# Kernel tuning notes

Hardware: AMD Instinct MI355X
Metric: run time of the kernel (lower is better)

## Reference

```python
import jax, jax.numpy as jnp
import numpy as np
import math

D_MODEL = 1024
N_HEADS = 16
D_KV = 64
NUM_BUCKETS = 32
MAX_DISTANCE = 128
BATCH = 4
SEQ = 2048


def _relative_position_bucket(relative_position, num_buckets=NUM_BUCKETS, max_distance=MAX_DISTANCE):
    # bidirectional=True (encoder)
    num_buckets //= 2
    relative_buckets = (relative_position > 0).astype(jnp.int32) * num_buckets
    rp = jnp.abs(relative_position)
    max_exact = num_buckets // 2
    is_small = rp < max_exact
    rp_safe = jnp.maximum(rp, 1)  # avoid log(0); masked by is_small anyway
    rp_if_large = max_exact + (
        jnp.log(rp_safe.astype(jnp.float32) / max_exact)
        / math.log(max_distance / max_exact)
        * (num_buckets - max_exact)
    ).astype(jnp.int32)
    rp_if_large = jnp.minimum(rp_if_large, num_buckets - 1)
    relative_buckets += jnp.where(is_small, rp, rp_if_large)
    return relative_buckets


def compute_bias(rel_bias, q_len, k_len):
    context = jnp.arange(q_len)[:, None]
    memory = jnp.arange(k_len)[None, :]
    buckets = _relative_position_bucket(memory - context)  # [q, k]
    values = rel_bias[buckets]                              # [q, k, h]
    return jnp.transpose(values, (2, 0, 1))[None]           # [1, h, q, k]


def setup_inputs() -> dict:
    key = jax.random.key(0)
    ks = jax.random.split(key, 6)
    s = 1.0 / math.sqrt(D_MODEL)
    return {
        "hidden_states": jax.random.normal(ks[0], (BATCH, SEQ, D_MODEL), jnp.float32),
        "wq": jax.random.normal(ks[1], (D_MODEL, N_HEADS * D_KV), jnp.float32) * s,
        "wk": jax.random.normal(ks[2], (D_MODEL, N_HEADS * D_KV), jnp.float32) * s,
        "wv": jax.random.normal(ks[3], (D_MODEL, N_HEADS * D_KV), jnp.float32) * s,
        "wo": jax.random.normal(ks[4], (N_HEADS * D_KV, D_MODEL), jnp.float32) * s,
        "rel_bias": jax.random.normal(ks[5], (NUM_BUCKETS, N_HEADS), jnp.float32) * 0.5,
    }


def reference(hidden_states, wq, wk, wv, wo, rel_bias):
    B, S, _ = hidden_states.shape

    def shape(x):  # [B,S,H*Dk] -> [B,H,S,Dk]
        return x.reshape(B, S, N_HEADS, D_KV).transpose(0, 2, 1, 3)

    q = shape(hidden_states @ wq)
    k = shape(hidden_states @ wk)
    v = shape(hidden_states @ wv)

    # NOTE: T5 does NOT scale by 1/sqrt(d_kv)
    scores = jnp.einsum("bhqd,bhkd->bhqk", q, k)
    position_bias = compute_bias(rel_bias, S, S)  # [1,H,S,S]
    scores = scores + position_bias
    attn = jax.nn.softmax(scores.astype(jnp.float32), axis=-1).astype(scores.dtype)
    ctx = jnp.einsum("bhqk,bhkd->bhqd", attn, v)
    ctx = ctx.transpose(0, 2, 1, 3).reshape(B, S, N_HEADS * D_KV)
    return ctx @ wo
```

## Files before the change

kernel.cpp:

```cpp
#include <hip/hip_runtime.h>
#include <hip/hip_bf16.h>

typedef unsigned short u16;
typedef unsigned int   u32;
typedef __bf16 bf16x8 __attribute__((ext_vector_type(8)));
typedef float  f32x4  __attribute__((ext_vector_type(4)));
typedef u16    u16x8  __attribute__((ext_vector_type(8)));
typedef u16    u16x4  __attribute__((ext_vector_type(4)));

#define MFMA16(a,b,c) __builtin_amdgcn_mfma_f32_16x16x32_bf16(a,b,c,0,0,0)
#define LOG2E 1.4426950408889634f

__device__ __forceinline__ u16 f2b(float f) {
    u32 u = __builtin_bit_cast(u32, f);
    u32 r = (u + 0x7FFFu + ((u >> 16) & 1u)) >> 16;
    return (u16)r;
}

typedef const __attribute__((address_space(1))) u32* gaddr_t;
typedef __attribute__((address_space(3))) u32*       laddr_t;
__device__ __forceinline__ void gl_lds16(const void* g, void* l) {
    __builtin_amdgcn_global_load_lds((gaddr_t)g, (laddr_t)l, 16, 0, 0);
}

__global__ __launch_bounds__(256) void prep_kernel(
        const float* __restrict__ H, const float* __restrict__ wq,
        const float* __restrict__ wk, const float* __restrict__ wv,
        const float* __restrict__ wo, const float* __restrict__ rel_bias,
        u16* __restrict__ Hb, u16* __restrict__ Wt, u16* __restrict__ Wot,
        float* __restrict__ tab) {
    __shared__ u16 tile[64 * 72];
    int bi = blockIdx.x;
    int t = threadIdx.x;
    if (bi < 4096) {
        int i = (bi * 256 + t) * 8;
        float4 a = *(const float4*)(H + i);
        float4 b = *(const float4*)(H + i + 4);
        u16x8 o = { f2b(a.x), f2b(a.y), f2b(a.z), f2b(a.w),
                    f2b(b.x), f2b(b.y), f2b(b.z), f2b(b.w) };
        *(u16x8*)(Hb + i) = o;
    } else if (bi < 5120) {
        int g2 = bi - 4096;
        int g = g2 >> 8, rem = g2 & 255;
        int n0 = (rem >> 4) * 64, k0 = (rem & 15) * 64;
        const float* src = (g == 0) ? wq : (g == 1) ? wk : (g == 2) ? wv : wo;
        u16* dst = (g < 3) ? (Wt + g * 1048576) : Wot;
#pragma unroll
        for (int rr = 0; rr < 4; ++rr) {
            int idx = rr * 256 + t;
            int kr = idx >> 4, c = idx & 15;
            float4 v = *(const float4*)(src + (k0 + kr) * 1024 + n0 + c * 4);
            u16x4 o = { f2b(v.x), f2b(v.y), f2b(v.z), f2b(v.w) };
            *(u16x4*)&tile[kr * 72 + c * 4] = o;
        }
        __syncthreads();
#pragma unroll
        for (int rr = 0; rr < 2; ++rr) {
            int idx = rr * 256 + t;
            int n = idx >> 3, c = idx & 7;
            u16x8 o;
#pragma unroll
            for (int j = 0; j < 8; ++j) o[j] = tile[(c * 8 + j) * 72 + n];
            *(u16x8*)(dst + (n0 + n) * 1024 + k0 + c * 8) = o;
        }
    } else {
        int i = (bi - 5120) * 256 + t;
        int h = i >> 12;
        int idx = i & 4095;
        int delta = idx - 2048;
        int bucket = (delta > 0) ? 16 : 0;
        int rp = delta < 0 ? -delta : delta;
        if (rp < 8) {
            bucket += rp;
        } else {
            double v = log((double)rp / 8.0) / log(16.0) * 8.0;
            int tt = (int)v;
            int b2 = 8 + tt;
            bucket += (b2 < 15) ? b2 : 15;
        }
        tab[h * 4096 + idx] = rel_bias[bucket * 16 + h] * LOG2E;
    }
}

template <int MODE>
__global__ __launch_bounds__(256) void gemm_bt(
        const u16* __restrict__ A, const u16* __restrict__ Bt, int K, int N,
        u16* __restrict__ q_out, u16* __restrict__ k_out, u16* __restrict__ v_out,
        float* __restrict__ f_out) {
    __shared__ u16 As[128 * 32];
    __shared__ u16 Bs[128 * 32];
    __shared__ u16 vt_tile[MODE == 0 ? 128 * 136 : 1];
    int t = threadIdx.x;
    int lane = t & 63, w = t >> 6;
    int wm = w & 1, wn = w >> 1;
    int ln = lane & 15, quad = lane >> 4;
    int m0 = blockIdx.x * 128, n0 = blockIdx.y * 128;
    const u16* Ab = A + m0 * K;
    const u16* Bb = Bt + n0 * K;
    f32x4 acc[4][4] = {};
    int nk = K >> 5;
    for (int kt = 0; kt < nk; ++kt) {
        int k0 = kt * 32;
#pragma unroll
        for (int rr = 0; rr < 2; ++rr) {
            int idx = rr * 256 + t;
            int row = idx >> 2, c = (idx & 3) ^ (row & 3);
            gl_lds16(Ab + row * K + k0 + c * 8, ((char*)As) + idx * 16);
            gl_lds16(Bb + row * K + k0 + c * 8, ((char*)Bs) + idx * 16);
        }
        __syncthreads();
        bf16x8 af[4], bfr[4];
#pragma unroll
        for (int mb = 0; mb < 4; ++mb) {
            int row = wm * 64 + mb * 16 + ln;
            af[mb] = *(const bf16x8*)&As[row * 32 + ((quad ^ (row & 3)) << 3)];
        }
#pragma unroll
        for (int nb = 0; nb < 4; ++nb) {
            int row = wn * 64 + nb * 16 + ln;
            bfr[nb] = *(const bf16x8*)&Bs[row * 32 + ((quad ^ (row & 3)) << 3)];
        }
#pragma unroll
        for (int mb = 0; mb < 4; ++mb)
#pragma unroll
            for (int nb = 0; nb < 4; ++nb)
                acc[mb][nb] = MFMA16(af[mb], bfr[nb], acc[mb][nb]);
        __syncthreads();
    }
    if (MODE == 0 && n0 >= 2048) {
#pragma unroll
        for (int mb = 0; mb < 4; ++mb)
#pragma unroll
            for (int nb = 0; nb < 4; ++nb)
#pragma unroll
                for (int r = 0; r < 4; ++r) {
                    int np = wn * 64 + nb * 16 + ln;
                    int mp = wm * 64 + mb * 16 + quad * 4 + r;
                    vt_tile[np * 136 + mp] = f2b(acc[mb][nb][r]);
                }
        __syncthreads();
        int h0 = (n0 >> 6) & 15;
        int b = m0 >> 11;
        int s0 = m0 & 2047;
#pragma unroll
        for (int j = 0; j < 8; ++j) {
            int e = j * 256 + t;
            int d_all = e >> 4;
            int sc = e & 15;
            int hh = h0 + (d_all >> 6);
            int d = d_all & 63;
            u16x8 val = *(const u16x8*)&vt_tile[d_all * 136 + sc * 8];
            *(u16x8*)(v_out + (b * 16 + hh) * 131072 + d * 2048 + s0 + sc * 8) = val;
        }
    } else {
#pragma unroll
        for (int mb = 0; mb < 4; ++mb)
#pragma unroll
            for (int nb = 0; nb < 4; ++nb)
#pragma unroll
                for (int r = 0; r < 4; ++r) {
                    int m = m0 + wm * 64 + mb * 16 + quad * 4 + r;
                    int n = n0 + wn * 64 + nb * 16 + ln;
                    float v = acc[mb][nb][r];
                    if (MODE == 0) {
                        int which = n >> 10, h = (n >> 6) & 15, d = n & 63;
                        int b = m >> 11, s = m & 2047;
                        u16* dst = (which == 0) ? q_out : k_out;
                        float scale = (which == 0) ? LOG2E : 1.0f;
                        dst[(((b << 4) + h) * 2048 + s) * 64 + d] = f2b(v * scale);
                    } else {
                        f_out[m * N + n] = v;
                    }
                }
    }
}

__global__ __launch_bounds__(256, 3) void attn_kernel(
        const u16* __restrict__ Qb, const u16* __restrict__ Kb,
        const u16* __restrict__ Vt, const float* __restrict__ bias_tab,
        u16* __restrict__ ctx) {
    __shared__ u16 Ks[2][64 * 64];
    __shared__ u16 Vs[2][64 * 64];
    __shared__ u16 Ps[4][16 * 64];
    __shared__ float sb[384];
    int t = threadIdx.x;
    int lane = t & 63, w = t >> 6;
    int ln = lane & 15, quad = lane >> 4;
    int bh = blockIdx.x >> 5;
    int qtile = blockIdx.x & 31;
    int h = bh & 15, b = bh >> 4;
    int q0 = qtile * 64;

    float chi = bias_tab[h * 4096 + 2048 + 1500];
    float clo = bias_tab[h * 4096 + 2048 - 1500];

    const float* tb = bias_tab + h * 4096 + 1857;
    for (int i = t; i < 384; i += 256) sb[i] = tb[i];

    int qa = q0 + w * 16 + ln;
    const u16* qptr = Qb + (bh * 2048 + qa) * 64 + quad * 8;
    bf16x8 qf0 = *(const bf16x8*)(qptr);
    bf16x8 qf1 = *(const bf16x8*)(qptr + 32);

    const u16* Kbase = Kb + bh * 2048 * 64;
    const u16* Vbase = Vt + bh * 64 * 2048;

    f32x4 oacc[4] = {};
    float l_i = 0.0f;
    int cb2_base = 191 - w * 16 + quad * 4 - ln;
    int swl = ln & 7;

#pragma unroll
    for (int it = 0; it < 2; ++it) {
        int idx = it * 256 + t;
        int row = idx >> 3, c = (idx & 7) ^ (row & 7);
        gl_lds16(Kbase + row * 64 + c * 8, ((char*)&Ks[0][0]) + idx * 16);
        gl_lds16(Vbase + row * 2048 + c * 8, ((char*)&Vs[0][0]) + idx * 16);
    }
    __syncthreads();

#pragma unroll 2
    for (int kt = 0; kt < 32; ++kt) {
        int cur = kt & 1;
        int kb0 = kt * 64;

        if (kt < 31) {
            int nxt = kb0 + 64;
#pragma unroll
            for (int it = 0; it < 2; ++it) {
                int idx = it * 256 + t;
                int row = idx >> 3, c = (idx & 7) ^ (row & 7);
                gl_lds16(Kbase + (nxt + row) * 64 + c * 8,
                         ((char*)&Ks[cur ^ 1][0]) + idx * 16);
                gl_lds16(Vbase + row * 2048 + nxt + c * 8,
                         ((char*)&Vs[cur ^ 1][0]) + idx * 16);
            }
        }
        const u16* Kc = &Ks[cur][0];
        const u16* Vc = &Vs[cur][0];

        f32x4 sacc[4];
        int diff = kb0 - q0;
        if (diff >= 192 || diff <= -192) {
            float c0 = (diff > 0) ? chi : clo;
            f32x4 ci = {c0, c0, c0, c0};
            __builtin_amdgcn_s_setprio(1);
#pragma unroll
            for (int nb = 0; nb < 4; ++nb) {
                int key = nb * 16 + ln;
                int sw = key & 7;
                bf16x8 kf0 = *(const bf16x8*)&Kc[key * 64 + ((quad ^ sw) << 3)];
                bf16x8 kf1 = *(const bf16x8*)&Kc[key * 64 + (((quad ^ 4) ^ sw) << 3)];
                f32x4 scc = MFMA16(kf0, qf0, ci);
                sacc[nb] = MFMA16(kf1, qf1, scc);
            }
            __builtin_amdgcn_s_setprio(0);
        } else {
            int cb = diff + cb2_base;
            __builtin_amdgcn_s_setprio(1);
#pragma unroll
            for (int nb = 0; nb < 4; ++nb) {
                int key = nb * 16 + ln;
                int sw = key & 7;
                const float* bp = &sb[cb + nb * 16];
                f32x4 ci = {bp[0], bp[1], bp[2], bp[3]};
                bf16x8 kf0 = *(const bf16x8*)&Kc[key * 64 + ((quad ^ sw) << 3)];
                bf16x8 kf1 = *(const bf16x8*)&Kc[key * 64 + (((quad ^ 4) ^ sw) << 3)];
                f32x4 scc = MFMA16(kf0, qf0, ci);
                sacc[nb] = MFMA16(kf1, qf1, scc);
            }
            __builtin_amdgcn_s_setprio(0);
        }

        float p[4][4];
        float ls0 = 0.f, ls1 = 0.f, ls2 = 0.f, ls3 = 0.f;
#pragma unroll
        for (int nb = 0; nb < 4; ++nb) {
            float e0 = __builtin_amdgcn_exp2f(sacc[nb][0]);
            float e1 = __builtin_amdgcn_exp2f(sacc[nb][1]);
            float e2 = __builtin_amdgcn_exp2f(sacc[nb][2]);
            float e3 = __builtin_amdgcn_exp2f(sacc[nb][3]);
            p[nb][0] = e0; p[nb][1] = e1; p[nb][2] = e2; p[nb][3] = e3;
            ls0 += e0; ls1 += e1; ls2 += e2; ls3 += e3;
        }
        l_i += (ls0 + ls1) + (ls2 + ls3);

        u16* pw = &Ps[w][0];
#pragma unroll
        for (int nb = 0; nb < 4; ++nb) {
            u32 lo, hi;
            asm("v_cvt_pk_bf16_f32 %0, %1, %2" : "=v"(lo) : "v"(p[nb][0]), "v"(p[nb][1]));
            asm("v_cvt_pk_bf16_f32 %0, %1, %2" : "=v"(hi) : "v"(p[nb][2]), "v"(p[nb][3]));
            int c = nb * 2 + (quad >> 1);
            u32* dst = (u32*)&pw[ln * 64 + ((c ^ swl) << 3) + (quad & 1) * 4];
            dst[0] = lo;
            dst[1] = hi;
        }

#pragma unroll
        for (int kc = 0; kc < 2; ++kc) {
            bf16x8 pf = *(const bf16x8*)&pw[ln * 64 + (((kc * 4 + quad) ^ swl) << 3)];
            __builtin_amdgcn_s_setprio(1);
#pragma unroll
            for (int nb = 0; nb < 4; ++nb) {
                int d = nb * 16 + ln;
                int vc = (kc * 4 + quad) ^ (d & 7);
                bf16x8 vf = *(const bf16x8*)&Vc[d * 64 + (vc << 3)];
                oacc[nb] = MFMA16(pf, vf, oacc[nb]);
            }
            __builtin_amdgcn_s_setprio(0);
        }
        __syncthreads();
    }

    l_i += __shfl_xor(l_i, 16);
    l_i += __shfl_xor(l_i, 32);
    float linv = 1.0f / l_i;
#pragma unroll
    for (int r = 0; r < 4; ++r) {
        float lr = __shfl(linv, quad * 4 + r);
        int q = q0 + w * 16 + quad * 4 + r;
#pragma unroll
        for (int nb = 0; nb < 4; ++nb)
            ctx[(b * 2048 + q) * 1024 + h * 64 + nb * 16 + ln] = f2b(oacc[nb][r] * lr);
    }
}

extern "C" void kernel_launch(void* const* d_in, const int* in_sizes, int n_in,
                              void* d_out, int out_size, void* d_ws, size_t ws_size,
                              hipStream_t stream) {
    const float* H   = (const float*)d_in[0];
    const float* wq  = (const float*)d_in[1];
    const float* wk  = (const float*)d_in[2];
    const float* wv  = (const float*)d_in[3];
    const float* wo  = (const float*)d_in[4];
    const float* rel = (const float*)d_in[5];
    float* out = (float*)d_out;

    char* ws = (char*)d_ws;
    u16* Hb    = (u16*)(ws);
    u16* Wt    = (u16*)(ws + 16777216);
    u16* Wot   = (u16*)(ws + 23068672);
    u16* Qb    = (u16*)(ws + 25165824);
    u16* Kb    = (u16*)(ws + 41943040);
    u16* Vt    = (u16*)(ws + 58720256);
    float* bias_tab = (float*)(ws + 75497472);
    u16* ctx = Hb;

    prep_kernel<<<5376, 256, 0, stream>>>(H, wq, wk, wv, wo, rel, Hb, Wt, Wot, bias_tab);
    gemm_bt<0><<<dim3(64, 24), 256, 0, stream>>>(Hb, Wt, 1024, 3072, Qb, Kb, Vt, nullptr);
    attn_kernel<<<2048, 256, 0, stream>>>(Qb, Kb, Vt, bias_tab, ctx);
    gemm_bt<1><<<dim3(64, 8), 256, 0, stream>>>(ctx, Wot, 1024, 1024, nullptr, nullptr, nullptr, out);
}
```

Before: 307.7 us.

## Overlap next K/V tile loads with compute using partial vmcnt waits

Restructures the flash-attention K/V double-buffer loop so the next tile's global-to-LDS loads are issued before waiting. A partial s_waitcnt vmcnt(4) then waits only for the current tile, replacing the full __syncthreads drain, so prefetch stays in flight during compute. The last tile is peeled out of the loop. Using a raw s_barrier without an LDS waitcnt risks subtle ordering issues, and the loop is no longer unrolled by 2.

```diff
diff --git a/kernel.cpp b/kernel.cpp
--- a/kernel.cpp
+++ b/kernel.cpp
@@ -210,35 +210,19 @@
     int cb2_base = 191 - w * 16 + quad * 4 - ln;
     int swl = ln & 7;
 
-#pragma unroll
-    for (int it = 0; it < 2; ++it) {
-        int idx = it * 256 + t;
-        int row = idx >> 3, c = (idx & 7) ^ (row & 7);
-        gl_lds16(Kbase + row * 64 + c * 8, ((char*)&Ks[0][0]) + idx * 16);
-        gl_lds16(Vbase + row * 2048 + c * 8, ((char*)&Vs[0][0]) + idx * 16);
-    }
-    __syncthreads();
-
-#pragma unroll 2
-    for (int kt = 0; kt < 32; ++kt) {
-        int cur = kt & 1;
-        int kb0 = kt * 64;
-
-        if (kt < 31) {
-            int nxt = kb0 + 64;
-#pragma unroll
-            for (int it = 0; it < 2; ++it) {
-                int idx = it * 256 + t;
-                int row = idx >> 3, c = (idx & 7) ^ (row & 7);
-                gl_lds16(Kbase + (nxt + row) * 64 + c * 8,
-                         ((char*)&Ks[cur ^ 1][0]) + idx * 16);
-                gl_lds16(Vbase + row * 2048 + nxt + c * 8,
-                         ((char*)&Vs[cur ^ 1][0]) + idx * 16);
-            }
-        }
-        const u16* Kc = &Ks[cur][0];
-        const u16* Vc = &Vs[cur][0];
-
+    auto stage = [&](int kb, int bufidx) {
+#pragma unroll
+        for (int it = 0; it < 2; ++it) {
+            int idx = it * 256 + t;
+            int row = idx >> 3, c = (idx & 7) ^ (row & 7);
+            gl_lds16(Kbase + (kb + row) * 64 + c * 8,
+                     ((char*)&Ks[bufidx][0]) + idx * 16);
+            gl_lds16(Vbase + row * 2048 + kb + c * 8,
+                     ((char*)&Vs[bufidx][0]) + idx * 16);
+        }
+    };
+
+    auto compute = [&](int kb0, const u16* Kc, const u16* Vc) {
         f32x4 sacc[4];
         int diff = kb0 - q0;
         if (diff >= 192 || diff <= -192) {
@@ -310,8 +294,22 @@
             }
             __builtin_amdgcn_s_setprio(0);
         }
-        __syncthreads();
-    }
+    };
+
+    stage(0, 0);
+    for (int kt = 0; kt < 31; ++kt) {
+        int cur = kt & 1;
+        stage((kt + 1) * 64, cur ^ 1);
+        asm volatile("s_waitcnt vmcnt(4)" ::: "memory");
+        __builtin_amdgcn_sched_barrier(0);
+        __builtin_amdgcn_s_barrier();
+        compute(kt * 64, &Ks[cur][0], &Vs[cur][0]);
+        __builtin_amdgcn_s_barrier();
+    }
+    asm volatile("s_waitcnt vmcnt(0)" ::: "memory");
+    __builtin_amdgcn_sched_barrier(0);
+    __builtin_amdgcn_s_barrier();
+    compute(31 * 64, &Ks[1][0], &Vs[1][0]);
 
     l_i += __shfl_xor(l_i, 16);
     l_i += __shfl_xor(l_i, 32);
```

After: 307.0 us. Within noise of the previous version (-0.2%).
